# Optimization experiments

Measured on AMD Instinct MI355X. Metric: run time of the kernel, lower is better.

## Reference

```python
import jax, jax.numpy as jnp
import numpy as np

B, L, M, K = 2, 2048, 16, 32
NUM_RBF = 16
MAX_REL = 32  # max_relative_feature in PositionalEncodings


def _linear(x, W, b):
    return x @ W.T + b


def _layernorm(x, g, b, eps=1e-5):
    mu = x.mean(-1, keepdims=True)
    var = ((x - mu) ** 2).mean(-1, keepdims=True)
    return (x - mu) * jax.lax.rsqrt(var + eps) * g + b


def _rbf(D):
    mu = jnp.linspace(2.0, 22.0, NUM_RBF)
    sigma = (22.0 - 2.0) / NUM_RBF
    return jnp.exp(-(((D[..., None] - mu) / sigma) ** 2))


def _gather_edges(feat, E_idx):
    # feat [B,L,L,C], E_idx [B,L,K] -> [B,L,K,C]
    return jnp.take_along_axis(feat, E_idx[..., None], axis=2)


def _dist(Xc, mask, eps=1e-6):
    mask2 = mask[:, :, None] * mask[:, None, :]
    dX = Xc[:, :, None, :] - Xc[:, None, :, :]
    D = mask2 * jnp.sqrt(jnp.sum(dX * dX, -1) + eps)
    D_max = jnp.max(D, -1, keepdims=True)
    D_adj = D + (1.0 - mask2) * D_max
    negD, E_idx = jax.lax.top_k(-D_adj, K)
    return -negD, E_idx


def _get_rbf(A, Bc, E_idx):
    D = jnp.sqrt(jnp.sum((A[:, :, None, :] - Bc[:, None, :, :]) ** 2, -1) + 1e-6)
    return _rbf(_gather_edges(D[..., None], E_idx)[..., 0])


def _angle_features(A, Bc, C, Y):
    v1, v2 = A - Bc, C - Bc
    e1 = v1 / (jnp.linalg.norm(v1, axis=-1, keepdims=True) + 1e-8)
    u2 = v2 - e1 * jnp.sum(e1 * v2, -1, keepdims=True)
    e2 = u2 / (jnp.linalg.norm(u2, axis=-1, keepdims=True) + 1e-8)
    e3 = jnp.cross(e1, e2)
    R = jnp.stack([e1, e2, e3], axis=-1)  # [B,L,3,3]
    lv = jnp.einsum('blqp,blyq->blyp', R, Y - Bc[:, :, None, :])
    rxy = jnp.sqrt(lv[..., 0] ** 2 + lv[..., 1] ** 2 + 1e-8)
    rxyz = jnp.linalg.norm(lv, axis=-1) + 1e-8
    return jnp.stack([lv[..., 0] / rxy, lv[..., 1] / rxy, rxy / rxyz, lv[..., 2] / rxyz], axis=-1)


def setup_inputs() -> dict:
    key = jax.random.key(0)
    ks = jax.random.split(key, 16)
    X = 10.0 * jax.random.normal(ks[0], (B, L, 4, 3), jnp.float32)
    Y = 10.0 * jax.random.normal(ks[1], (B, L, M, 3), jnp.float32)
    Y_t = jax.random.randint(ks[2], (B, L, M), 0, 120)
    Y_m = jnp.ones((B, L, M), jnp.float32)
    mask = jnp.ones((B, L), jnp.float32)
    R_idx = jnp.tile(jnp.arange(L, dtype=jnp.int32)[None], (B, 1))
    chain_labels = jax.random.randint(ks[3], (B, L), 0, 4)
    periodic_table = jnp.stack([
        jnp.arange(120, dtype=jnp.int32),
        jax.random.randint(ks[4], (120,), 0, 19),  # group
        jax.random.randint(ks[5], (120,), 0, 8),   # period
    ])
    s = 0.05
    def w(k, shape):
        return s * jax.random.normal(k, shape, jnp.float32)
    return dict(
        X=X, Y=Y, Y_m=Y_m, mask=mask,
        W_pos=w(ks[6], (16, 66)), b_pos=jnp.zeros(16),
        W_edge=w(ks[7], (128, 416)), b_edge=jnp.zeros(128),
        g_edge=jnp.ones(128), be_edge=jnp.zeros(128),
        W_down=w(ks[8], (128, 148)), b_down=jnp.zeros(128),
        g_node=jnp.ones(128), bn_node=jnp.zeros(128),
        W_type=w(ks[9], (64, 147)), b_type=jnp.zeros(64),
        W_yn=w(ks[10], (128, 147)), b_yn=jnp.zeros(128),
        g_yn=jnp.ones(128), bn_yn=jnp.zeros(128),
        W_ye=w(ks[11], (128, 16)), b_ye=jnp.zeros(128),
        g_ye=jnp.ones(128), bn_ye=jnp.zeros(128),
        Y_t=Y_t, R_idx=R_idx, chain_labels=chain_labels, periodic_table=periodic_table)


def reference(X, Y, Y_m, mask, W_pos, b_pos, W_edge, b_edge, g_edge, be_edge,
              W_down, b_down, g_node, bn_node, W_type, b_type,
              W_yn, b_yn, g_yn, bn_yn, W_ye, b_ye, g_ye, bn_ye,
              Y_t, R_idx, chain_labels, periodic_table):
    N = X[:, :, 0, :]; Ca = X[:, :, 1, :]; C = X[:, :, 2, :]; O = X[:, :, 3, :]
    b_ = Ca - N; c_ = C - Ca; a_ = jnp.cross(b_, c_)
    Cb = -0.58273431 * a_ + 0.56802827 * b_ - 0.54067466 * c_ + Ca
    D_neighbors, E_idx = _dist(Ca, mask)
    pairs = [(N, N), (C, C), (O, O), (Cb, Cb), (Ca, N), (Ca, C), (Ca, O), (Ca, Cb),
             (N, C), (N, O), (N, Cb), (Cb, C), (Cb, O), (O, C), (N, Ca), (C, Ca),
             (O, Ca), (Cb, Ca), (C, N), (O, N), (Cb, N), (C, Cb), (O, Cb), (C, O)]
    RBF_all = jnp.concatenate([_rbf(D_neighbors)] + [_get_rbf(a, bb, E_idx) for a, bb in pairs], axis=-1)
    offset = _gather_edges((R_idx[:, :, None] - R_idx[:, None, :])[..., None], E_idx)[..., 0]
    d_chains = (chain_labels[:, :, None] == chain_labels[:, None, :]).astype(jnp.int32)
    E_chains = _gather_edges(d_chains[..., None], E_idx)[..., 0]
    d = jnp.clip(offset + MAX_REL, 0, 2 * MAX_REL) * E_chains + (1 - E_chains) * (2 * MAX_REL + 1)
    E_pos = _linear(jax.nn.one_hot(d, 2 * MAX_REL + 2, dtype=jnp.float32), W_pos, b_pos)
    E = _layernorm(_linear(jnp.concatenate([E_pos, RBF_all], -1), W_edge, b_edge), g_edge, be_edge)
    Y_t = Y_t.astype(jnp.int32)
    Y_t_1hot_full = jnp.concatenate([
        jax.nn.one_hot(Y_t, 120, dtype=jnp.float32),
        jax.nn.one_hot(periodic_table[1][Y_t], 19, dtype=jnp.float32),
        jax.nn.one_hot(periodic_table[2][Y_t], 8, dtype=jnp.float32)], -1)
    Y_t_proj = _linear(Y_t_1hot_full, W_type, b_type)
    def rbf_to_Y(A):
        return _rbf(jnp.sqrt(jnp.sum((A[:, :, None, :] - Y) ** 2, -1) + 1e-6))
    f_angles = _angle_features(N, Ca, C, Y)
    D_all = jnp.concatenate([rbf_to_Y(N), rbf_to_Y(Ca), rbf_to_Y(C), rbf_to_Y(O), rbf_to_Y(Cb), Y_t_proj, f_angles], -1)
    V = _layernorm(_linear(D_all, W_down, b_down), g_node, bn_node)
    Y_edges = _rbf(jnp.sqrt(jnp.sum((Y[:, :, :, None, :] - Y[:, :, None, :, :]) ** 2, -1) + 1e-6))
    Y_edges = _layernorm(_linear(Y_edges, W_ye, b_ye), g_ye, bn_ye)
    Y_nodes = _layernorm(_linear(Y_t_1hot_full, W_yn, b_yn), g_yn, bn_yn)
    return (V, E, E_idx, Y_nodes, Y_edges, Y_m)
```

## Files before the change

kernel.cpp:

```cpp
#include <hip/hip_runtime.h>
#include <math.h>

#define BB 2
#define LL 2048
#define MM 16
#define KNN 32

#define OFF_V    0
#define OFF_E    8388608
#define OFF_EIDX 25165824
#define OFF_YN   25296896
#define OFF_YE   33685504
#define OFF_YM   167903232

__device__ const int PAIR_A[24] = {0,2,3,4,1,1,1,1,0,0,0,4,4,3,0,2,3,4,2,3,4,2,3,2};
__device__ const int PAIR_B[24] = {0,2,3,4,0,2,3,4,2,3,4,2,3,2,1,1,1,1,0,0,0,4,4,3};

__global__ __launch_bounds__(256) void prep_kernel(
    const float* __restrict__ Wedge, const float* __restrict__ Wdown,
    const float* __restrict__ X,
    float* __restrict__ WtE, float* __restrict__ WtD, float* __restrict__ Cb)
{
    int idx = blockIdx.x * 256 + threadIdx.x;
    if (idx < 53248) {
        int f = idx >> 7, c = idx & 127;
        WtE[idx] = Wedge[c * 416 + f];
    } else if (idx < 53248 + 18944) {
        int k = idx - 53248;
        int f = k >> 7, c = k & 127;
        WtD[k] = Wdown[c * 148 + f];
    } else if (idx < 53248 + 18944 + BB * LL) {
        int r = idx - 53248 - 18944;
        float Nx = X[r*12+0], Ny = X[r*12+1], Nz = X[r*12+2];
        float Ax = X[r*12+3], Ay = X[r*12+4], Az = X[r*12+5];
        float Cx = X[r*12+6], Cy = X[r*12+7], Cz = X[r*12+8];
        float bx = Ax - Nx, by = Ay - Ny, bz = Az - Nz;
        float cx = Cx - Ax, cy = Cy - Ay, cz = Cz - Az;
        float ax = by * cz - bz * cy;
        float ay = bz * cx - bx * cz;
        float az = bx * cy - by * cx;
        Cb[r*3+0] = -0.58273431f*ax + 0.56802827f*bx - 0.54067466f*cx + Ax;
        Cb[r*3+1] = -0.58273431f*ay + 0.56802827f*by - 0.54067466f*cy + Ay;
        Cb[r*3+2] = -0.58273431f*az + 0.56802827f*bz - 0.54067466f*cz + Az;
    }
}

__global__ __launch_bounds__(256) void knn_kernel(
    const float* __restrict__ X, const float* __restrict__ mask,
    int* __restrict__ eidx, float* __restrict__ dn, float* __restrict__ out)
{
    const int row = blockIdx.x;
    const int t = threadIdx.x;
    const int b = row >> 11;
    __shared__ float dist[LL];
    __shared__ float rv[256];
    __shared__ int   ri[256];

    const float cx = X[row*12+3], cy = X[row*12+4], cz = X[row*12+5];
    const float mi = mask[row];
    float lmax = -1e30f;
    for (int s = 0; s < LL/256; ++s) {
        int j = s*256 + t;
        int gj = b*LL + j;
        float dx = cx - X[gj*12+3];
        float dy = cy - X[gj*12+4];
        float dz = cz - X[gj*12+5];
        float D = mi * mask[gj] * sqrtf(dx*dx + dy*dy + dz*dz + 1e-6f);
        dist[j] = D;
        lmax = fmaxf(lmax, D);
    }
    rv[t] = lmax;
    __syncthreads();
    for (int off = 128; off > 0; off >>= 1) {
        if (t < off) rv[t] = fmaxf(rv[t], rv[t+off]);
        __syncthreads();
    }
    const float Dmax = rv[0];
    __syncthreads();
    for (int s = 0; s < LL/256; ++s) {
        int j = s*256 + t;
        int gj = b*LL + j;
        float m2 = mi * mask[gj];
        dist[j] = dist[j] + (1.0f - m2) * Dmax;
    }
    __syncthreads();
    for (int sel = 0; sel < KNN; ++sel) {
        float bv = 1e30f; int bi = -1;
        for (int s = 0; s < LL/256; ++s) {
            int j = s*256 + t;
            float v = dist[j];
            if (v < bv) { bv = v; bi = j; }
        }
        rv[t] = bv; ri[t] = bi;
        __syncthreads();
        for (int off = 128; off > 0; off >>= 1) {
            if (t < off) {
                float v2 = rv[t+off]; int i2 = ri[t+off];
                if (v2 < rv[t] || (v2 == rv[t] && i2 < ri[t])) { rv[t] = v2; ri[t] = i2; }
            }
            __syncthreads();
        }
        if (t == 0) {
            int bj = ri[0];
            eidx[row*KNN + sel] = bj;
            dn[row*KNN + sel] = rv[0];
            out[OFF_EIDX + row*KNN + sel] = (float)bj;
            dist[bj] = 1e30f;
        }
        __syncthreads();
    }
}

__global__ __launch_bounds__(256) void edge_kernel(
    const float* __restrict__ X, const float* __restrict__ Cb,
    const int* __restrict__ Ridx, const int* __restrict__ chains,
    const float* __restrict__ Wpos, const float* __restrict__ bpos,
    const float* __restrict__ Wt, const float* __restrict__ bedge,
    const float* __restrict__ ge, const float* __restrict__ be,
    const int* __restrict__ eidx, const float* __restrict__ dn,
    float* __restrict__ out)
{
    const int row = blockIdx.x;
    const int t = threadIdx.x;
    const int b = row >> 11;
    __shared__ __attribute__((aligned(16))) float smem[KNN*420];
    float (*feat)[420] = (float(*)[420])smem;
    float (*o)[129] = (float(*)[129])smem;
    __shared__ float jat[KNN][15];
    __shared__ float dd[KNN][25];
    __shared__ float iat[15];
    __shared__ int   jd[KNN];
    __shared__ float stat[KNN][2];

    if (t < 12) iat[t] = X[row*12 + t];
    else if (t < 15) iat[t] = Cb[row*3 + (t-12)];
    if (t < KNN) {
        int j = eidx[row*KNN + t];
        int gj = b*LL + j;
        #pragma unroll
        for (int q = 0; q < 12; ++q) jat[t][q] = X[gj*12 + q];
        jat[t][12] = Cb[gj*3+0];
        jat[t][13] = Cb[gj*3+1];
        jat[t][14] = Cb[gj*3+2];
        int off = Ridx[row] - Ridx[gj];
        int dcl = off + 32;
        dcl = dcl < 0 ? 0 : (dcl > 64 ? 64 : dcl);
        jd[t] = (chains[row] == chains[gj]) ? dcl : 65;
        dd[t][0] = dn[row*KNN + t];
    }
    __syncthreads();
    for (int idx = t; idx < 24*KNN; idx += 256) {
        int k = idx & (KNN-1);
        int gp = idx >> 5;
        int a = PAIR_A[gp], b2 = PAIR_B[gp];
        float dx = iat[a*3+0] - jat[k][b2*3+0];
        float dy = iat[a*3+1] - jat[k][b2*3+1];
        float dz = iat[a*3+2] - jat[k][b2*3+2];
        dd[k][gp+1] = sqrtf(dx*dx + dy*dy + dz*dz + 1e-6f);
    }
    __syncthreads();
    for (int idx = t; idx < KNN*400; idx += 256) {
        int k = idx / 400;
        int f = idx - k*400;
        float d = dd[k][f >> 4];
        int r = f & 15;
        float z = (d - (2.0f + 1.3333333333f*(float)r)) * 0.8f;
        feat[k][16 + f] = expf(-z*z);
    }
    for (int idx = t; idx < KNN*16; idx += 256) {
        int k = idx >> 4, p = idx & 15;
        feat[k][p] = Wpos[p*66 + jd[k]] + bpos[p];
    }
    __syncthreads();
    const int c2 = (t & 63) * 2;
    const int g4 = t >> 6;
    float acc[8][2];
    #pragma unroll
    for (int r = 0; r < 8; ++r) { acc[r][0] = bedge[c2]; acc[r][1] = bedge[c2+1]; }
    for (int f = 0; f < 416; f += 4) {
        const float2 w0 = *(const float2*)&Wt[(f+0)*128 + c2];
        const float2 w1 = *(const float2*)&Wt[(f+1)*128 + c2];
        const float2 w2 = *(const float2*)&Wt[(f+2)*128 + c2];
        const float2 w3 = *(const float2*)&Wt[(f+3)*128 + c2];
        #pragma unroll
        for (int r = 0; r < 8; ++r) {
            const float4 fv = *(const float4*)&feat[g4*8 + r][f];
            acc[r][0] = fmaf(fv.x, w0.x, acc[r][0]);
            acc[r][0] = fmaf(fv.y, w1.x, acc[r][0]);
            acc[r][0] = fmaf(fv.z, w2.x, acc[r][0]);
            acc[r][0] = fmaf(fv.w, w3.x, acc[r][0]);
            acc[r][1] = fmaf(fv.x, w0.y, acc[r][1]);
            acc[r][1] = fmaf(fv.y, w1.y, acc[r][1]);
            acc[r][1] = fmaf(fv.z, w2.y, acc[r][1]);
            acc[r][1] = fmaf(fv.w, w3.y, acc[r][1]);
        }
    }
    __syncthreads();
    #pragma unroll
    for (int r = 0; r < 8; ++r) {
        o[g4*8 + r][c2]   = acc[r][0];
        o[g4*8 + r][c2+1] = acc[r][1];
    }
    __syncthreads();
    if (t < KNN) {
        float s = 0.0f;
        for (int c = 0; c < 128; ++c) s += o[t][c];
        float mu = s * 0.0078125f;
        float v = 0.0f;
        for (int c = 0; c < 128; ++c) { float d = o[t][c] - mu; v = fmaf(d, d, v); }
        stat[t][0] = mu;
        stat[t][1] = rsqrtf(v * 0.0078125f + 1e-5f);
    }
    __syncthreads();
    const size_t base = (size_t)OFF_E + (size_t)row * KNN * 128;
    for (int idx = t; idx < KNN*128; idx += 256) {
        int k = idx >> 7, c = idx & 127;
        out[base + idx] = (o[k][c] - stat[k][0]) * stat[k][1] * ge[c] + be[c];
    }
}

__global__ __launch_bounds__(256) void node_kernel(
    const float* __restrict__ X, const float* __restrict__ CbA,
    const float* __restrict__ Yp, const int* __restrict__ Yt,
    const int* __restrict__ ptab,
    const float* __restrict__ Wtype, const float* __restrict__ btype,
    const float* __restrict__ WtD, const float* __restrict__ bdown,
    const float* __restrict__ gnode, const float* __restrict__ bnnode,
    const float* __restrict__ Wyn, const float* __restrict__ byn,
    const float* __restrict__ gyn, const float* __restrict__ bnyn,
    float* __restrict__ out)
{
    const int row = blockIdx.x;
    const int t = threadIdx.x;
    __shared__ float atoms[5][3];
    __shared__ float evec[3][3];
    __shared__ float Ys[MM][3];
    __shared__ float dst[5][MM];
    __shared__ __attribute__((aligned(16))) float feat[MM][152];
    __shared__ float o[MM][129];
    __shared__ float stat[MM][2];
    __shared__ int tinfo[MM][3];

    if (t < 12) atoms[t/3][t%3] = X[row*12 + t];
    else if (t < 15) atoms[4][t-12] = CbA[row*3 + (t-12)];
    if (t >= 16 && t < 64) { int q = t - 16; Ys[q/3][q%3] = Yp[row*48 + q]; }
    if (t >= 64 && t < 80) {
        int m = t - 64;
        int ty = Yt[row*16 + m];
        tinfo[m][0] = ty;
        tinfo[m][1] = ptab[120 + ty];
        tinfo[m][2] = ptab[240 + ty];
    }
    __syncthreads();
    if (t == 0) {
        float v1x = atoms[0][0]-atoms[1][0], v1y = atoms[0][1]-atoms[1][1], v1z = atoms[0][2]-atoms[1][2];
        float v2x = atoms[2][0]-atoms[1][0], v2y = atoms[2][1]-atoms[1][1], v2z = atoms[2][2]-atoms[1][2];
        float n1 = sqrtf(v1x*v1x + v1y*v1y + v1z*v1z) + 1e-8f;
        float e1x = v1x/n1, e1y = v1y/n1, e1z = v1z/n1;
        float dp = e1x*v2x + e1y*v2y + e1z*v2z;
        float u2x = v2x - e1x*dp, u2y = v2y - e1y*dp, u2z = v2z - e1z*dp;
        float n2 = sqrtf(u2x*u2x + u2y*u2y + u2z*u2z) + 1e-8f;
        float e2x = u2x/n2, e2y = u2y/n2, e2z = u2z/n2;
        evec[0][0] = e1x; evec[0][1] = e1y; evec[0][2] = e1z;
        evec[1][0] = e2x; evec[1][1] = e2y; evec[1][2] = e2z;
        evec[2][0] = e1y*e2z - e1z*e2y;
        evec[2][1] = e1z*e2x - e1x*e2z;
        evec[2][2] = e1x*e2y - e1y*e2x;
    }
    if (t >= 128 && t < 208) {
        int q = t - 128;
        int a = q >> 4, m = q & 15;
        float dx = atoms[a][0]-Ys[m][0];
        float dy = atoms[a][1]-Ys[m][1];
        float dz = atoms[a][2]-Ys[m][2];
        dst[a][m] = sqrtf(dx*dx + dy*dy + dz*dz + 1e-6f);
    }
    __syncthreads();
    for (int idx = t; idx < 5*16*16; idx += 256) {
        int a = idx >> 8, m = (idx >> 4) & 15, r = idx & 15;
        float z = (dst[a][m] - (2.0f + 1.3333333333f*(float)r)) * 0.8f;
        feat[m][a*16 + r] = expf(-z*z);
    }
    for (int idx = t; idx < 1024; idx += 256) {
        int m = idx >> 6, c = idx & 63;
        const float* wr = Wtype + c*147;
        feat[m][80 + c] = wr[tinfo[m][0]] + wr[120 + tinfo[m][1]] + wr[139 + tinfo[m][2]] + btype[c];
    }
    if (t < 16) {
        int m = t;
        float dx = Ys[m][0]-atoms[1][0], dy = Ys[m][1]-atoms[1][1], dz = Ys[m][2]-atoms[1][2];
        float l0 = evec[0][0]*dx + evec[0][1]*dy + evec[0][2]*dz;
        float l1 = evec[1][0]*dx + evec[1][1]*dy + evec[1][2]*dz;
        float l2 = evec[2][0]*dx + evec[2][1]*dy + evec[2][2]*dz;
        float rxy  = sqrtf(l0*l0 + l1*l1 + 1e-8f);
        float rxyz = sqrtf(l0*l0 + l1*l1 + l2*l2) + 1e-8f;
        feat[m][144] = l0 / rxy;
        feat[m][145] = l1 / rxy;
        feat[m][146] = rxy / rxyz;
        feat[m][147] = l2 / rxyz;
    }
    __syncthreads();
    const int c2 = (t & 63) * 2;
    const int g4 = t >> 6;
    float acc[4][2];
    #pragma unroll
    for (int r = 0; r < 4; ++r) { acc[r][0] = bdown[c2]; acc[r][1] = bdown[c2+1]; }
    for (int f = 0; f < 148; f += 4) {
        const float2 w0 = *(const float2*)&WtD[(f+0)*128 + c2];
        const float2 w1 = *(const float2*)&WtD[(f+1)*128 + c2];
        const float2 w2 = *(const float2*)&WtD[(f+2)*128 + c2];
        const float2 w3 = *(const float2*)&WtD[(f+3)*128 + c2];
        #pragma unroll
        for (int r = 0; r < 4; ++r) {
            const float4 fv = *(const float4*)&feat[g4*4 + r][f];
            acc[r][0] = fmaf(fv.x, w0.x, acc[r][0]);
            acc[r][0] = fmaf(fv.y, w1.x, acc[r][0]);
            acc[r][0] = fmaf(fv.z, w2.x, acc[r][0]);
            acc[r][0] = fmaf(fv.w, w3.x, acc[r][0]);
            acc[r][1] = fmaf(fv.x, w0.y, acc[r][1]);
            acc[r][1] = fmaf(fv.y, w1.y, acc[r][1]);
            acc[r][1] = fmaf(fv.z, w2.y, acc[r][1]);
            acc[r][1] = fmaf(fv.w, w3.y, acc[r][1]);
        }
    }
    #pragma unroll
    for (int r = 0; r < 4; ++r) {
        o[g4*4 + r][c2]   = acc[r][0];
        o[g4*4 + r][c2+1] = acc[r][1];
    }
    __syncthreads();
    if (t < 16) {
        float s = 0.0f;
        for (int c = 0; c < 128; ++c) s += o[t][c];
        float mu = s * 0.0078125f;
        float v = 0.0f;
        for (int c = 0; c < 128; ++c) { float d = o[t][c] - mu; v = fmaf(d, d, v); }
        stat[t][0] = mu;
        stat[t][1] = rsqrtf(v * 0.0078125f + 1e-5f);
    }
    __syncthreads();
    const size_t vbase = (size_t)OFF_V + (size_t)row * 2048;
    for (int idx = t; idx < 2048; idx += 256) {
        int k = idx >> 7, c = idx & 127;
        out[vbase + idx] = (o[k][c] - stat[k][0]) * stat[k][1] * gnode[c] + bnnode[c];
    }
    __syncthreads();
    for (int idx = t; idx < 2048; idx += 256) {
        int m = idx >> 7, c = idx & 127;
        const float* wr = Wyn + c*147;
        o[m][c] = wr[tinfo[m][0]] + wr[120 + tinfo[m][1]] + wr[139 + tinfo[m][2]] + byn[c];
    }
    __syncthreads();
    if (t < 16) {
        float s = 0.0f;
        for (int c = 0; c < 128; ++c) s += o[t][c];
        float mu = s * 0.0078125f;
        float v = 0.0f;
        for (int c = 0; c < 128; ++c) { float d = o[t][c] - mu; v = fmaf(d, d, v); }
        stat[t][0] = mu;
        stat[t][1] = rsqrtf(v * 0.0078125f + 1e-5f);
    }
    __syncthreads();
    const size_t ybase = (size_t)OFF_YN + (size_t)row * 2048;
    for (int idx = t; idx < 2048; idx += 256) {
        int k = idx >> 7, c = idx & 127;
        out[ybase + idx] = (o[k][c] - stat[k][0]) * stat[k][1] * gyn[c] + bnyn[c];
    }
}

__global__ __launch_bounds__(256) void yedge_kernel(
    const float* __restrict__ Yp, const float* __restrict__ Wye,
    const float* __restrict__ bye, const float* __restrict__ gye,
    const float* __restrict__ bnye, float* __restrict__ out)
{
    const int blk = blockIdx.x;
    const int row = blk >> 2;
    const int r0 = (blk & 3) * 64;
    const int t = threadIdx.x;
    __shared__ float Ys[MM][3];
    __shared__ __attribute__((aligned(16))) float Wt[16][128];
    __shared__ __attribute__((aligned(16))) float feat[64][20];
    __shared__ float o[64][129];
    __shared__ float stat[64][2];

    if (t < 48) Ys[t/3][t%3] = Yp[row*48 + t];
    for (int idx = t; idx < 2048; idx += 256) {
        int c = idx & 127, f = idx >> 7;
        Wt[f][c] = Wye[c*16 + f];
    }
    __syncthreads();
    for (int idx = t; idx < 64*16; idx += 256) {
        int r = idx >> 4, rr = idx & 15;
        int gr = r0 + r;
        int m1 = gr >> 4, m2 = gr & 15;
        float dx = Ys[m1][0]-Ys[m2][0];
        float dy = Ys[m1][1]-Ys[m2][1];
        float dz = Ys[m1][2]-Ys[m2][2];
        float d = sqrtf(dx*dx + dy*dy + dz*dz + 1e-6f);
        float z = (d - (2.0f + 1.3333333333f*(float)rr)) * 0.8f;
        feat[r][rr] = expf(-z*z);
    }
    __syncthreads();
    const int c2 = (t & 63) * 2;
    const int g4 = t >> 6;
    float acc[16][2];
    #pragma unroll
    for (int r = 0; r < 16; ++r) { acc[r][0] = bye[c2]; acc[r][1] = bye[c2+1]; }
    #pragma unroll
    for (int f = 0; f < 16; f += 4) {
        const float2 w0 = *(const float2*)&Wt[f+0][c2];
        const float2 w1 = *(const float2*)&Wt[f+1][c2];
        const float2 w2 = *(const float2*)&Wt[f+2][c2];
        const float2 w3 = *(const float2*)&Wt[f+3][c2];
        #pragma unroll
        for (int r = 0; r < 16; ++r) {
            const float4 fv = *(const float4*)&feat[g4*16 + r][f];
            acc[r][0] = fmaf(fv.x, w0.x, acc[r][0]);
            acc[r][0] = fmaf(fv.y, w1.x, acc[r][0]);
            acc[r][0] = fmaf(fv.z, w2.x, acc[r][0]);
            acc[r][0] = fmaf(fv.w, w3.x, acc[r][0]);
            acc[r][1] = fmaf(fv.x, w0.y, acc[r][1]);
            acc[r][1] = fmaf(fv.y, w1.y, acc[r][1]);
            acc[r][1] = fmaf(fv.z, w2.y, acc[r][1]);
            acc[r][1] = fmaf(fv.w, w3.y, acc[r][1]);
        }
    }
    #pragma unroll
    for (int r = 0; r < 16; ++r) {
        o[g4*16 + r][c2]   = acc[r][0];
        o[g4*16 + r][c2+1] = acc[r][1];
    }
    __syncthreads();
    if (t < 64) {
        float s = 0.0f;
        for (int c = 0; c < 128; ++c) s += o[t][c];
        float mu = s * 0.0078125f;
        float v = 0.0f;
        for (int c = 0; c < 128; ++c) { float d = o[t][c] - mu; v = fmaf(d, d, v); }
        stat[t][0] = mu;
        stat[t][1] = rsqrtf(v * 0.0078125f + 1e-5f);
    }
    __syncthreads();
    const size_t base = (size_t)OFF_YE + ((size_t)row * 256 + r0) * 128;
    for (int idx = t; idx < 64*128; idx += 256) {
        int k = idx >> 7, c = idx & 127;
        out[base + idx] = (o[k][c] - stat[k][0]) * stat[k][1] * gye[c] + bnye[c];
    }
}

extern "C" void kernel_launch(void* const* d_in, const int* in_sizes, int n_in,
                              void* d_out, int out_size, void* d_ws, size_t ws_size,
                              hipStream_t stream) {
    (void)in_sizes; (void)n_in; (void)out_size; (void)ws_size;
    const float* X      = (const float*)d_in[0];
    const float* Y      = (const float*)d_in[1];
    const float* Y_m    = (const float*)d_in[2];
    const float* mask   = (const float*)d_in[3];
    const float* W_pos  = (const float*)d_in[4];
    const float* b_pos  = (const float*)d_in[5];
    const float* W_edge = (const float*)d_in[6];
    const float* b_edge = (const float*)d_in[7];
    const float* g_edge = (const float*)d_in[8];
    const float* be_edge= (const float*)d_in[9];
    const float* W_down = (const float*)d_in[10];
    const float* b_down = (const float*)d_in[11];
    const float* g_node = (const float*)d_in[12];
    const float* bn_node= (const float*)d_in[13];
    const float* W_type = (const float*)d_in[14];
    const float* b_type = (const float*)d_in[15];
    const float* W_yn   = (const float*)d_in[16];
    const float* b_yn   = (const float*)d_in[17];
    const float* g_yn   = (const float*)d_in[18];
    const float* bn_yn  = (const float*)d_in[19];
    const float* W_ye   = (const float*)d_in[20];
    const float* b_ye   = (const float*)d_in[21];
    const float* g_ye   = (const float*)d_in[22];
    const float* bn_ye  = (const float*)d_in[23];
    const int* Y_t      = (const int*)d_in[24];
    const int* R_idx    = (const int*)d_in[25];
    const int* chains   = (const int*)d_in[26];
    const int* ptab     = (const int*)d_in[27];

    float* out = (float*)d_out;
    float* ws  = (float*)d_ws;
    float* WtE = ws;
    float* WtD = ws + 53248;
    float* Cb  = ws + 72192;
    int*   eidx = (int*)(ws + 84480);
    float* dn  = ws + 215552;

    prep_kernel<<<298, 256, 0, stream>>>(W_edge, W_down, X, WtE, WtD, Cb);
    knn_kernel<<<BB*LL, 256, 0, stream>>>(X, mask, eidx, dn, out);
    edge_kernel<<<BB*LL, 256, 0, stream>>>(X, Cb, R_idx, chains, W_pos, b_pos,
                                           WtE, b_edge, g_edge, be_edge, eidx, dn, out);
    node_kernel<<<BB*LL, 256, 0, stream>>>(X, Cb, Y, Y_t, ptab, W_type, b_type,
                                           WtD, b_down, g_node, bn_node,
                                           W_yn, b_yn, g_yn, bn_yn, out);
    yedge_kernel<<<BB*LL*4, 256, 0, stream>>>(Y, W_ye, b_ye, g_ye, bn_ye, out);
    hipMemcpyAsync(out + OFF_YM, Y_m, (size_t)BB*LL*MM*sizeof(float),
                   hipMemcpyDeviceToDevice, stream);
}
```

Baseline: 1.273 ms.

## Register-resident packed-key top-k in knn and shuffle-based layernorm stats

The knn kernel now keeps each thread's 8 distances in registers as packed 64-bit (distance, index) keys. Each selection round rescans only the one wavefront that held the previous winner, using wave shuffles and a double-buffered per-wave minimum, instead of a full 256-thread shared-memory tree reduction with many barriers. Ca coordinates and mask are packed into float4 staging in the Y_edges output region, which yedge_kernel overwrites later. Layernorm statistics in all kernels are computed by all 256 threads with shuffle reductions rather than a few serial threads looping over 128 columns. The packed-key ordering relies on distances being non-negative for the float-bit comparison.

```diff
diff --git a/kernel.cpp b/kernel.cpp
--- a/kernel.cpp
+++ b/kernel.cpp
@@ -16,10 +16,35 @@
 __device__ const int PAIR_A[24] = {0,2,3,4,1,1,1,1,0,0,0,4,4,3,0,2,3,4,2,3,4,2,3,2};
 __device__ const int PAIR_B[24] = {0,2,3,4,0,2,3,4,2,3,4,2,3,2,1,1,1,1,0,0,0,4,4,3};
 
+template<int R>
+__device__ inline void ln_stats(const float (*o)[129], float (*stat)[2], int t)
+{
+    constexpr int G = 256 / R;
+    constexpr int C = 128 / G;
+    const int k = t / G, sub = t % G;
+    const float* orow = o[k];
+    float s = 0.0f;
+    #pragma unroll
+    for (int c = 0; c < C; ++c) s += orow[c*G + sub];
+    #pragma unroll
+    for (int off = G/2; off > 0; off >>= 1) s += __shfl_xor(s, off, 64);
+    const float mu = s * 0.0078125f;
+    float v = 0.0f;
+    #pragma unroll
+    for (int c = 0; c < C; ++c) { float d = orow[c*G + sub] - mu; v = fmaf(d, d, v); }
+    #pragma unroll
+    for (int off = G/2; off > 0; off >>= 1) v += __shfl_xor(v, off, 64);
+    if (sub == 0) {
+        stat[k][0] = mu;
+        stat[k][1] = rsqrtf(v * 0.0078125f + 1e-5f);
+    }
+}
+
 __global__ __launch_bounds__(256) void prep_kernel(
     const float* __restrict__ Wedge, const float* __restrict__ Wdown,
-    const float* __restrict__ X,
-    float* __restrict__ WtE, float* __restrict__ WtD, float* __restrict__ Cb)
+    const float* __restrict__ X, const float* __restrict__ mask,
+    float* __restrict__ WtE, float* __restrict__ WtD, float* __restrict__ Cb,
+    float4* __restrict__ CaM)
 {
     int idx = blockIdx.x * 256 + threadIdx.x;
     if (idx < 53248) {
@@ -42,72 +67,97 @@
         Cb[r*3+0] = -0.58273431f*ax + 0.56802827f*bx - 0.54067466f*cx + Ax;
         Cb[r*3+1] = -0.58273431f*ay + 0.56802827f*by - 0.54067466f*cy + Ay;
         Cb[r*3+2] = -0.58273431f*az + 0.56802827f*bz - 0.54067466f*cz + Az;
+    } else if (idx < 53248 + 18944 + 2 * BB * LL) {
+        int r = idx - 53248 - 18944 - BB * LL;
+        float4 v;
+        v.x = X[r*12+3]; v.y = X[r*12+4]; v.z = X[r*12+5]; v.w = mask[r];
+        CaM[r] = v;
     }
 }
 
 __global__ __launch_bounds__(256) void knn_kernel(
-    const float* __restrict__ X, const float* __restrict__ mask,
+    const float4* __restrict__ CaM,
     int* __restrict__ eidx, float* __restrict__ dn, float* __restrict__ out)
 {
     const int row = blockIdx.x;
     const int t = threadIdx.x;
     const int b = row >> 11;
-    __shared__ float dist[LL];
-    __shared__ float rv[256];
-    __shared__ int   ri[256];
-
-    const float cx = X[row*12+3], cy = X[row*12+4], cz = X[row*12+5];
-    const float mi = mask[row];
+    const int lane = t & 63;
+    const int wid = t >> 6;
+
+    __shared__ float wmaxs[4];
+    __shared__ unsigned long long wmin[2][4];
+
+    const float4 me = CaM[row];
+    float dd[8];
+    float m2v[8];
     float lmax = -1e30f;
-    for (int s = 0; s < LL/256; ++s) {
-        int j = s*256 + t;
-        int gj = b*LL + j;
-        float dx = cx - X[gj*12+3];
-        float dy = cy - X[gj*12+4];
-        float dz = cz - X[gj*12+5];
-        float D = mi * mask[gj] * sqrtf(dx*dx + dy*dy + dz*dz + 1e-6f);
-        dist[j] = D;
+    #pragma unroll
+    for (int s = 0; s < 8; ++s) {
+        float4 o4 = CaM[b*LL + s*256 + t];
+        float dx = me.x - o4.x, dy = me.y - o4.y, dz = me.z - o4.z;
+        float m2 = me.w * o4.w;
+        float D = m2 * sqrtf(dx*dx + dy*dy + dz*dz + 1e-6f);
+        dd[s] = D;
+        m2v[s] = m2;
         lmax = fmaxf(lmax, D);
     }
-    rv[t] = lmax;
-    __syncthreads();
-    for (int off = 128; off > 0; off >>= 1) {
-        if (t < off) rv[t] = fmaxf(rv[t], rv[t+off]);
+    #pragma unroll
+    for (int off = 32; off > 0; off >>= 1)
+        lmax = fmaxf(lmax, __shfl_xor(lmax, off, 64));
+    if (lane == 0) wmaxs[wid] = lmax;
+    __syncthreads();
+    const float Dmax = fmaxf(fmaxf(wmaxs[0], wmaxs[1]), fmaxf(wmaxs[2], wmaxs[3]));
+
+    unsigned long long key[8];
+    unsigned long long lmin = ~0ull;
+    #pragma unroll
+    for (int s = 0; s < 8; ++s) {
+        float adj = fmaf(1.0f - m2v[s], Dmax, dd[s]);
+        key[s] = ((unsigned long long)__float_as_uint(adj) << 32)
+               | (unsigned long long)(unsigned)(s*256 + t);
+        lmin = key[s] < lmin ? key[s] : lmin;
+    }
+    unsigned long long wm = lmin;
+    #pragma unroll
+    for (int off = 32; off > 0; off >>= 1) {
+        unsigned long long o = __shfl_xor(wm, off, 64);
+        wm = o < wm ? o : wm;
+    }
+    if (lane == 0) wmin[0][wid] = wm;
+    __syncthreads();
+
+    int p = 0;
+    for (int sel = 0; sel < KNN; ++sel) {
+        unsigned long long g = wmin[p][0];
+        g = wmin[p][1] < g ? wmin[p][1] : g;
+        g = wmin[p][2] < g ? wmin[p][2] : g;
+        g = wmin[p][3] < g ? wmin[p][3] : g;
+        if (t == 0) {
+            int j = (int)(g & 0x7ff);
+            eidx[row*KNN + sel] = j;
+            dn[row*KNN + sel] = __uint_as_float((unsigned)(g >> 32));
+            out[OFF_EIDX + row*KNN + sel] = (float)j;
+        }
+        if (sel == KNN - 1) break;
+        const int jwin = (int)(g & 0x7ff);
+        const int wwid = (jwin & 255) >> 6;
+        if (wid == wwid) {
+            #pragma unroll
+            for (int s = 0; s < 8; ++s) key[s] = (key[s] == g) ? ~0ull : key[s];
+            unsigned long long m = key[0];
+            #pragma unroll
+            for (int s = 1; s < 8; ++s) m = key[s] < m ? key[s] : m;
+            #pragma unroll
+            for (int off = 32; off > 0; off >>= 1) {
+                unsigned long long o = __shfl_xor(m, off, 64);
+                m = o < m ? o : m;
+            }
+            wm = m;
+        }
+        if (lane == 0) wmin[p^1][wid] = wm;
         __syncthreads();
-    }
-    const float Dmax = rv[0];
-    __syncthreads();
-    for (int s = 0; s < LL/256; ++s) {
-        int j = s*256 + t;
-        int gj = b*LL + j;
-        float m2 = mi * mask[gj];
-        dist[j] = dist[j] + (1.0f - m2) * Dmax;
-    }
-    __syncthreads();
-    for (int sel = 0; sel < KNN; ++sel) {
-        float bv = 1e30f; int bi = -1;
-        for (int s = 0; s < LL/256; ++s) {
-            int j = s*256 + t;
-            float v = dist[j];
-            if (v < bv) { bv = v; bi = j; }
-        }
-        rv[t] = bv; ri[t] = bi;
-        __syncthreads();
-        for (int off = 128; off > 0; off >>= 1) {
-            if (t < off) {
-                float v2 = rv[t+off]; int i2 = ri[t+off];
-                if (v2 < rv[t] || (v2 == rv[t] && i2 < ri[t])) { rv[t] = v2; ri[t] = i2; }
-            }
-            __syncthreads();
-        }
-        if (t == 0) {
-            int bj = ri[0];
-            eidx[row*KNN + sel] = bj;
-            dn[row*KNN + sel] = rv[0];
-            out[OFF_EIDX + row*KNN + sel] = (float)bj;
-            dist[bj] = 1e30f;
-        }
-        __syncthreads();
+        p ^= 1;
     }
 }
 
@@ -202,15 +252,7 @@
         o[g4*8 + r][c2+1] = acc[r][1];
     }
     __syncthreads();
-    if (t < KNN) {
-        float s = 0.0f;
-        for (int c = 0; c < 128; ++c) s += o[t][c];
-        float mu = s * 0.0078125f;
-        float v = 0.0f;
-        for (int c = 0; c < 128; ++c) { float d = o[t][c] - mu; v = fmaf(d, d, v); }
-        stat[t][0] = mu;
-        stat[t][1] = rsqrtf(v * 0.0078125f + 1e-5f);
-    }
+    ln_stats<KNN>(o, stat, t);
     __syncthreads();
     const size_t base = (size_t)OFF_E + (size_t)row * KNN * 128;
     for (int idx = t; idx < KNN*128; idx += 256) {
@@ -329,15 +371,7 @@
         o[g4*4 + r][c2+1] = acc[r][1];
     }
     __syncthreads();
-    if (t < 16) {
-        float s = 0.0f;
-        for (int c = 0; c < 128; ++c) s += o[t][c];
-        float mu = s * 0.0078125f;
-        float v = 0.0f;
-        for (int c = 0; c < 128; ++c) { float d = o[t][c] - mu; v = fmaf(d, d, v); }
-        stat[t][0] = mu;
-        stat[t][1] = rsqrtf(v * 0.0078125f + 1e-5f);
-    }
+    ln_stats<MM>(o, stat, t);
     __syncthreads();
     const size_t vbase = (size_t)OFF_V + (size_t)row * 2048;
     for (int idx = t; idx < 2048; idx += 256) {
@@ -351,15 +385,7 @@
         o[m][c] = wr[tinfo[m][0]] + wr[120 + tinfo[m][1]] + wr[139 + tinfo[m][2]] + byn[c];
     }
     __syncthreads();
-    if (t < 16) {
-        float s = 0.0f;
-        for (int c = 0; c < 128; ++c) s += o[t][c];
-        float mu = s * 0.0078125f;
-        float v = 0.0f;
-        for (int c = 0; c < 128; ++c) { float d = o[t][c] - mu; v = fmaf(d, d, v); }
-        stat[t][0] = mu;
-        stat[t][1] = rsqrtf(v * 0.0078125f + 1e-5f);
-    }
+    ln_stats<MM>(o, stat, t);
     __syncthreads();
     const size_t ybase = (size_t)OFF_YN + (size_t)row * 2048;
     for (int idx = t; idx < 2048; idx += 256) {
@@ -431,15 +457,7 @@
         o[g4*16 + r][c2+1] = acc[r][1];
     }
     __syncthreads();
-    if (t < 64) {
-        float s = 0.0f;
-        for (int c = 0; c < 128; ++c) s += o[t][c];
-        float mu = s * 0.0078125f;
-        float v = 0.0f;
-        for (int c = 0; c < 128; ++c) { float d = o[t][c] - mu; v = fmaf(d, d, v); }
-        stat[t][0] = mu;
-        stat[t][1] = rsqrtf(v * 0.0078125f + 1e-5f);
-    }
+    ln_stats<64>(o, stat, t);
     __syncthreads();
     const size_t base = (size_t)OFF_YE + ((size_t)row * 256 + r0) * 128;
     for (int idx = t; idx < 64*128; idx += 256) {
@@ -489,8 +507,11 @@
     int*   eidx = (int*)(ws + 84480);
     float* dn  = ws + 215552;
 
-    prep_kernel<<<298, 256, 0, stream>>>(W_edge, W_down, X, WtE, WtD, Cb);
-    knn_kernel<<<BB*LL, 256, 0, stream>>>(X, mask, eidx, dn, out);
+    float* CaM = out + OFF_YE;
+
+    prep_kernel<<<314, 256, 0, stream>>>(W_edge, W_down, X, mask, WtE, WtD, Cb,
+                                         (float4*)CaM);
+    knn_kernel<<<BB*LL, 256, 0, stream>>>((const float4*)CaM, eidx, dn, out);
     edge_kernel<<<BB*LL, 256, 0, stream>>>(X, Cb, R_idx, chains, W_pos, b_pos,
                                            WtE, b_edge, g_edge, be_edge, eidx, dn, out);
     node_kernel<<<BB*LL, 256, 0, stream>>>(X, Cb, Y, Y_t, ptab, W_type, b_type,
```

After: 1.182 ms. 1.08x faster.
